# Kernel optimization log

Measured on AMD Instinct MI355X. Metric: run time of the kernel, lower is better.

## Reference

```python
import jax, jax.numpy as jnp
import numpy as np

N = 65536          # flattened input vectors
K = 2048           # num_embeddings (codebook size)
D = 128            # embedding_dim
COMMITMENT_COST = 1.0
DECAY = 0.99
EPS = 1e-05


def setup_inputs() -> dict:
    key = jax.random.key(0)
    k1, k2, k3 = jax.random.split(key, 3)
    inputs = jax.random.normal(k1, (N, D), dtype=jnp.float32)
    embedding = jax.random.normal(k2, (K, D), dtype=jnp.float32) * 0.01
    cluster_size = jnp.zeros((K,), dtype=jnp.float32)
    embed_avg = jax.random.normal(k3, (K, D), dtype=jnp.float32) * 0.01
    return {"inputs": inputs, "embedding": embedding,
            "cluster_size": cluster_size, "embed_avg": embed_avg}


def reference(inputs, embedding, cluster_size, embed_avg):
    input_shape = inputs.shape
    flat = inputs.reshape(-1, D)                                   # [N, D]

    # squared-L2 distances to codebook: [N, K]
    distances = (jnp.sum(flat ** 2, axis=1, keepdims=True)
                 + jnp.sum(embedding ** 2, axis=1)
                 - 2.0 * flat @ embedding.T)
    encoding_indices = jnp.argmin(distances, axis=1)               # [N] int

    quantized = embedding[encoding_indices].reshape(input_shape)   # gather

    # EMA codebook update (training mode). one-hot @ X expressed as segment sums.
    dw = jax.ops.segment_sum(jnp.ones((flat.shape[0],), flat.dtype),
                             encoding_indices, num_segments=K)      # [K]
    new_cluster_size = cluster_size * DECAY + (1.0 - DECAY) * dw
    dw_embed = jax.ops.segment_sum(flat, encoding_indices, num_segments=K)  # [K, D]
    new_embed_avg = embed_avg * DECAY + (1.0 - DECAY) * dw_embed
    n = new_cluster_size.sum()
    smoothed = (new_cluster_size + EPS) / (n + K * EPS) * n
    new_embedding = new_embed_avg / smoothed[:, None]

    # losses (detach == stop_gradient)
    e_latent_loss = jnp.mean((jax.lax.stop_gradient(quantized) - inputs) ** 2)
    q_latent_loss = jnp.mean((quantized - jax.lax.stop_gradient(inputs)) ** 2)
    loss = q_latent_loss + COMMITMENT_COST * e_latent_loss

    # straight-through estimator
    quantized_st = inputs + jax.lax.stop_gradient(quantized - inputs)
    return (quantized_st, loss, encoding_indices,
            new_embedding, new_cluster_size, new_embed_avg)
```

## Files before the change

### kernel.cpp

```cpp
#include <hip/hip_runtime.h>

#define NROWS 65536
#define KCODE 2048
#define DDIM  128

static constexpr float DECAYF = 0.99f;
static constexpr float OMDF   = (float)(1.0 - 0.99);
static constexpr float EPSF   = 1e-5f;
static constexpr float KEPSF  = (float)(2048.0 * 1e-5);
static constexpr float MARGIN = 1e-3f;

typedef __attribute__((ext_vector_type(8))) short bf16x8;
typedef __attribute__((ext_vector_type(4))) float f32x4;

__device__ __forceinline__ unsigned int bf16_rne_bits(float f) {
  unsigned int u = __builtin_bit_cast(unsigned int, f);
  return (u + 0x7fffu + ((u >> 16) & 1u)) >> 16;
}

__global__ __launch_bounds__(256) void k_split(const float* __restrict__ emb,
                                               unsigned short* __restrict__ ehi,
                                               unsigned short* __restrict__ elo) {
  int i = blockIdx.x * 256 + threadIdx.x;
  float f = emb[i];
  unsigned int hr = bf16_rne_bits(f);
  float hif = __builtin_bit_cast(float, hr << 16);
  float lo = f - hif;
  unsigned int lr = bf16_rne_bits(lo);
  ehi[i] = (unsigned short)hr;
  elo[i] = (unsigned short)lr;
}

__global__ __launch_bounds__(256) void k_sumsq_emb(const float* __restrict__ emb,
                                                   float* __restrict__ se) {
#pragma clang fp contract(off)
  int k = blockIdx.x * 256 + threadIdx.x;
  if (k >= KCODE) return;
  const float* row = emb + (size_t)k * DDIM;
  float s = 0.f;
#pragma unroll
  for (int d = 0; d < DDIM; ++d) {
    float q = row[d] * row[d];
    s = s + q;
  }
  se[k] = s;
}

__global__ __launch_bounds__(256, 2) void k_screen(
    const float* __restrict__ x, const unsigned short* __restrict__ ehi,
    const unsigned short* __restrict__ elo, const float* __restrict__ se,
    float* __restrict__ out_idxf, int* __restrict__ idx,
    int* __restrict__ flaglist, int* __restrict__ flagcnt) {
  const int tid = threadIdx.x;
  const int lane = tid & 63;
  const int wid = tid >> 6;
  const int rowbase = (blockIdx.x * 4 + wid) * 32;
  const int l15 = lane & 15, l4 = lane >> 4;

  __shared__ __align__(16) char lds[2][8192];
  char* lbase = &lds[0][0];

  bf16x8 ahi0[4], alo0[4], ahi1[4], alo1[4];
#pragma unroll
  for (int t = 0; t < 2; ++t) {
#pragma unroll
    for (int f = 0; f < 4; ++f) {
      const float4* s4 =
          (const float4*)(x + (size_t)(rowbase + t * 16 + l15) * DDIM + f * 32 + l4 * 8);
      float4 v0 = s4[0], v1 = s4[1];
      float fv[8] = {v0.x, v0.y, v0.z, v0.w, v1.x, v1.y, v1.z, v1.w};
      union { unsigned short u[8]; bf16x8 v; } H, L;
#pragma unroll
      for (int j = 0; j < 8; ++j) {
        unsigned int hr = bf16_rne_bits(fv[j]);
        float hif = __builtin_bit_cast(float, hr << 16);
        unsigned int lr = bf16_rne_bits(fv[j] - hif);
        H.u[j] = (unsigned short)hr;
        L.u[j] = (unsigned short)lr;
      }
      if (t == 0) { ahi0[f] = H.v; alo0[f] = L.v; }
      else        { ahi1[f] = H.v; alo1[f] = L.v; }
    }
  }

  int raddr[2][4];
#pragma unroll
  for (int p = 0; p < 2; ++p)
#pragma unroll
    for (int f = 0; f < 4; ++f)
      raddr[p][f] = p * 4096 + ((l15 * 256 + f * 64 + l4 * 16) ^ ((l15 & 7) << 4));

  const unsigned short* splane = (tid & 128) ? elo : ehi;
  const int po0 = (tid & 127) * 32;
  const char* sp = (const char*)splane + po0;
  const int wplane = (tid >> 7) * 4096;
  const int waddr0 = wplane + (po0 ^ (((po0 >> 8) & 7) << 4));
  const int waddr1 = wplane + ((po0 + 16) ^ ((((po0 + 16) >> 8) & 7) << 4));

  float m1[8], m2[8];
  int k1[8];
#pragma unroll
  for (int s = 0; s < 8; ++s) { m1[s] = INFINITY; m2[s] = INFINITY; k1[s] = 0; }

  {
    int4 v0 = *(const int4*)(sp);
    int4 v1 = *(const int4*)(sp + 16);
    *(int4*)(lbase + waddr0) = v0;
    *(int4*)(lbase + waddr1) = v1;
  }
  __syncthreads();

  int bufoff = 0;
#pragma unroll 2
  for (int g = 0; g < 128; ++g) {
    float sec = se[g * 16 + l15];
    int4 nv0, nv1;
    if (g < 127) {
      nv0 = *(const int4*)(sp + (size_t)(g + 1) * 4096);
      nv1 = *(const int4*)(sp + (size_t)(g + 1) * 4096 + 16);
    }
    f32x4 hh0 = {0.f, 0.f, 0.f, 0.f}, hl0 = {0.f, 0.f, 0.f, 0.f}, lh0 = {0.f, 0.f, 0.f, 0.f};
    f32x4 hh1 = {0.f, 0.f, 0.f, 0.f}, hl1 = {0.f, 0.f, 0.f, 0.f}, lh1 = {0.f, 0.f, 0.f, 0.f};
#pragma unroll
    for (int f = 0; f < 4; ++f) {
      bf16x8 BH = *(const bf16x8*)(lbase + bufoff + raddr[0][f]);
      bf16x8 BL = *(const bf16x8*)(lbase + bufoff + raddr[1][f]);
      hh0 = __builtin_amdgcn_mfma_f32_16x16x32_bf16(ahi0[f], BH, hh0, 0, 0, 0);
      lh0 = __builtin_amdgcn_mfma_f32_16x16x32_bf16(alo0[f], BH, lh0, 0, 0, 0);
      hl0 = __builtin_amdgcn_mfma_f32_16x16x32_bf16(ahi0[f], BL, hl0, 0, 0, 0);
      hh1 = __builtin_amdgcn_mfma_f32_16x16x32_bf16(ahi1[f], BH, hh1, 0, 0, 0);
      lh1 = __builtin_amdgcn_mfma_f32_16x16x32_bf16(alo1[f], BH, lh1, 0, 0, 0);
      hl1 = __builtin_amdgcn_mfma_f32_16x16x32_bf16(ahi1[f], BL, hl1, 0, 0, 0);
    }
    int c_ = g * 16 + l15;
#pragma unroll
    for (int s = 0; s < 4; ++s) {
      float vv = fmaf(-2.f, (hh0[s] + hl0[s]) + lh0[s], sec);
      m2[s] = fminf(m2[s], fmaxf(vv, m1[s]));
      k1[s] = (vv < m1[s]) ? c_ : k1[s];
      m1[s] = fminf(m1[s], vv);
      float vw = fmaf(-2.f, (hh1[s] + hl1[s]) + lh1[s], sec);
      m2[s + 4] = fminf(m2[s + 4], fmaxf(vw, m1[s + 4]));
      k1[s + 4] = (vw < m1[s + 4]) ? c_ : k1[s + 4];
      m1[s + 4] = fminf(m1[s + 4], vw);
    }
    if (g < 127) {
      *(int4*)(lbase + (bufoff ^ 8192) + waddr0) = nv0;
      *(int4*)(lbase + (bufoff ^ 8192) + waddr1) = nv1;
    }
    __syncthreads();
    bufoff ^= 8192;
  }

#pragma unroll
  for (int off = 1; off < 16; off <<= 1) {
#pragma unroll
    for (int s = 0; s < 8; ++s) {
      float om1 = __shfl_xor(m1[s], off);
      float om2 = __shfl_xor(m2[s], off);
      int ok1 = __shfl_xor(k1[s], off);
      m2[s] = fminf(fminf(m2[s], om2), fmaxf(m1[s], om1));
      k1[s] = (om1 < m1[s]) ? ok1 : k1[s];
      m1[s] = fminf(m1[s], om1);
    }
  }
  if (l15 == 0) {
#pragma unroll
    for (int s = 0; s < 8; ++s) {
      int row = rowbase + (s >> 2) * 16 + l4 * 4 + (s & 3);
      idx[row] = k1[s];
      out_idxf[row] = (float)k1[s];
      if (m2[s] - m1[s] <= MARGIN) {
        int p = atomicAdd(flagcnt, 1);
        if (p < NROWS) flaglist[p] = row;
      }
    }
  }
}

__global__ __launch_bounds__(64) void k_exact(
    const float* __restrict__ x, const float* __restrict__ emb,
    const float* __restrict__ se, const int* __restrict__ flaglist,
    const int* __restrict__ flagcnt, int* __restrict__ idx,
    float* __restrict__ out_idxf) {
#pragma clang fp contract(off)
  int cnt = *flagcnt;
  if (cnt > NROWS) cnt = NROWS;
  int lane = threadIdx.x;
  for (int i = blockIdx.x; i < cnt; i += gridDim.x) {
    int row = flaglist[i];
    const float4* xp = (const float4*)(x + (size_t)row * DDIM);
    float4 xr[32];
#pragma unroll
    for (int j = 0; j < 32; ++j) xr[j] = xp[j];
    float sx = 0.f;
#pragma unroll
    for (int j = 0; j < 32; ++j) {
      float q0 = xr[j].x * xr[j].x; sx = sx + q0;
      float q1 = xr[j].y * xr[j].y; sx = sx + q1;
      float q2 = xr[j].z * xr[j].z; sx = sx + q2;
      float q3 = xr[j].w * xr[j].w; sx = sx + q3;
    }
    float bestd = INFINITY;
    int bestk = lane * 32;
    for (int cb = 0; cb < 32; cb += 4) {
      float c4[4] = {0.f, 0.f, 0.f, 0.f};
#pragma unroll
      for (int d4 = 0; d4 < 32; ++d4) {
#pragma unroll
        for (int u = 0; u < 4; ++u) {
          float4 e = ((const float4*)(emb + (size_t)(lane * 32 + cb + u) * DDIM))[d4];
          c4[u] = fmaf(e.x, xr[d4].x, c4[u]);
          c4[u] = fmaf(e.y, xr[d4].y, c4[u]);
          c4[u] = fmaf(e.z, xr[d4].z, c4[u]);
          c4[u] = fmaf(e.w, xr[d4].w, c4[u]);
        }
      }
#pragma unroll
      for (int u = 0; u < 4; ++u) {
        int c = lane * 32 + cb + u;
        float t = sx + se[c];
        float tw = 2.0f * c4[u];
        float d = t - tw;
        if (d < bestd) { bestd = d; bestk = c; }
      }
    }
#pragma unroll
    for (int off = 1; off < 64; off <<= 1) {
      float od = __shfl_xor(bestd, off);
      int ok = __shfl_xor(bestk, off);
      if (od < bestd || (od == bestd && ok < bestk)) { bestd = od; bestk = ok; }
    }
    if (lane == 0) { idx[row] = bestk; out_idxf[row] = (float)bestk; }
  }
}

__global__ __launch_bounds__(256) void k_hist(const int* __restrict__ idx,
                                              int* __restrict__ cnt) {
  int n = blockIdx.x * 256 + threadIdx.x;
  atomicAdd(&cnt[idx[n]], 1);
}

__global__ __launch_bounds__(1024) void k_scan(const int* __restrict__ cnt,
                                               int* __restrict__ off,
                                               int* __restrict__ pos_ctr,
                                               float* __restrict__ dwf) {
  __shared__ int sA[2048], sB[2048];
  int t = threadIdx.x;
  int c0 = cnt[t], c1 = cnt[t + 1024];
  sA[t] = c0; sA[t + 1024] = c1;
  __syncthreads();
  int* src = sA; int* dst = sB;
  for (int o = 1; o < 2048; o <<= 1) {
    int v0 = src[t] + ((t >= o) ? src[t - o] : 0);
    int p1 = t + 1024;
    int v1 = src[p1] + ((p1 >= o) ? src[p1 - o] : 0);
    dst[t] = v0; dst[p1] = v1;
    __syncthreads();
    int* tmp = src; src = dst; dst = tmp;
  }
  int e0 = src[t] - c0;
  int e1 = src[t + 1024] - c1;
  off[t] = e0; off[t + 1024] = e1;
  pos_ctr[t] = e0; pos_ctr[t + 1024] = e1;
  dwf[t] = (float)c0; dwf[t + 1024] = (float)c1;
}

__global__ __launch_bounds__(256) void k_scatter(const int* __restrict__ idx,
                                                 int* __restrict__ pos_ctr,
                                                 int* __restrict__ rowlist) {
  int n = blockIdx.x * 256 + threadIdx.x;
  int k = idx[n];
  int p = atomicAdd(&pos_ctr[k], 1);
  rowlist[p] = n;
}

__global__ __launch_bounds__(128) void k_dwe(const float* __restrict__ x,
                                             const int* __restrict__ rowlist,
                                             const int* __restrict__ cnt,
                                             const int* __restrict__ off,
                                             float* __restrict__ dwe) {
  int k = blockIdx.x, d = threadIdx.x;
  int n = cnt[k], base = off[k];
  float s0 = 0.f, s1 = 0.f, s2 = 0.f, s3 = 0.f;
  int i = 0;
  for (; i + 4 <= n; i += 4) {
    int r0 = rowlist[base + i + 0];
    int r1 = rowlist[base + i + 1];
    int r2 = rowlist[base + i + 2];
    int r3 = rowlist[base + i + 3];
    s0 += x[(size_t)r0 * DDIM + d];
    s1 += x[(size_t)r1 * DDIM + d];
    s2 += x[(size_t)r2 * DDIM + d];
    s3 += x[(size_t)r3 * DDIM + d];
  }
  for (; i < n; ++i) {
    int r = rowlist[base + i];
    s0 += x[(size_t)r * DDIM + d];
  }
  dwe[(size_t)k * DDIM + d] = (s0 + s1) + (s2 + s3);
}

__global__ __launch_bounds__(256) void k_quant2(const float* __restrict__ x,
                                                const float* __restrict__ emb,
                                                const int* __restrict__ idx,
                                                float* __restrict__ out_q,
                                                double* __restrict__ partial_loss) {
#pragma clang fp contract(off)
  int t = blockIdx.x * 256 + threadIdx.x;
  int n = t >> 5, j = t & 31;
  int k = idx[n];
  float4 xv = ((const float4*)(x + (size_t)n * DDIM))[j];
  float4 ev = ((const float4*)(emb + (size_t)k * DDIM))[j];
  float d0 = ev.x - xv.x, d1 = ev.y - xv.y, d2 = ev.z - xv.z, d3 = ev.w - xv.w;
  float4 q;
  q.x = xv.x + d0; q.y = xv.y + d1; q.z = xv.z + d2; q.w = xv.w + d3;
  ((float4*)(out_q + (size_t)n * DDIM))[j] = q;

  float s = d0 * d0 + d1 * d1 + d2 * d2 + d3 * d3;
#pragma unroll
  for (int o = 32; o > 0; o >>= 1) s += __shfl_down(s, o);
  __shared__ float wsum[4];
  if ((threadIdx.x & 63) == 0) wsum[threadIdx.x >> 6] = s;
  __syncthreads();
  if (threadIdx.x == 0)
    partial_loss[blockIdx.x] =
        (double)((wsum[0] + wsum[1]) + (wsum[2] + wsum[3]));
}

__global__ __launch_bounds__(1024) void k_final1(const float* __restrict__ cs,
                                                 const float* __restrict__ dwf,
                                                 float* __restrict__ out_ncs,
                                                 float* __restrict__ smoothed,
                                                 const double* __restrict__ partial_loss,
                                                 float* __restrict__ out_loss) {
#pragma clang fp contract(off)
  __shared__ float red[1024];
  __shared__ double dred[1024];
  int t = threadIdx.x;
  float p0 = cs[t] * DECAYF;
  float p1 = cs[t + 1024] * DECAYF;
  float w0 = OMDF * dwf[t];
  float w1 = OMDF * dwf[t + 1024];
  float ncs0 = p0 + w0;
  float ncs1 = p1 + w1;
  out_ncs[t] = ncs0;
  out_ncs[t + 1024] = ncs1;
  red[t] = ncs0 + ncs1;
  double ds = 0.0;
#pragma unroll
  for (int i = 0; i < 8; ++i) ds += partial_loss[t + i * 1024];
  dred[t] = ds;
  __syncthreads();
  for (int o = 512; o > 0; o >>= 1) {
    if (t < o) { red[t] += red[t + o]; dred[t] += dred[t + o]; }
    __syncthreads();
  }
  float nsum = red[0];
  smoothed[t] = (ncs0 + EPSF) / (nsum + KEPSF) * nsum;
  smoothed[t + 1024] = (ncs1 + EPSF) / (nsum + KEPSF) * nsum;
  if (t == 0) {
    float m = (float)(dred[0] / (double)((size_t)NROWS * DDIM));
    out_loss[0] = m + 1.0f * m;
  }
}

__global__ __launch_bounds__(256) void k_final2(const float* __restrict__ ea,
                                                const float* __restrict__ dwe,
                                                const float* __restrict__ smoothed,
                                                float* __restrict__ out_ne,
                                                float* __restrict__ out_nea) {
#pragma clang fp contract(off)
  int i = blockIdx.x * 256 + threadIdx.x;
  float p = ea[i] * DECAYF;
  float w = OMDF * dwe[i];
  float nea = p + w;
  out_nea[i] = nea;
  out_ne[i] = nea / smoothed[i >> 7];
}

extern "C" void kernel_launch(void* const* d_in, const int* in_sizes, int n_in,
                              void* d_out, int out_size, void* d_ws, size_t ws_size,
                              hipStream_t stream) {
  const float* x   = (const float*)d_in[0];
  const float* emb = (const float*)d_in[1];
  const float* cs  = (const float*)d_in[2];
  const float* ea  = (const float*)d_in[3];

  float* out = (float*)d_out;
  float* out_q    = out;
  float* out_loss = out + 8388608;
  float* out_idx  = out + 8388609;
  float* out_ne   = out + 8454145;
  float* out_ncs  = out + 8716289;
  float* out_nea  = out + 8718337;

  char* ws = (char*)d_ws;
  unsigned short* ehi = (unsigned short*)(ws + 0);
  unsigned short* elo = (unsigned short*)(ws + 524288);
  int*    idx      = (int*)(ws + 1048576);
  int*    flaglist = (int*)(ws + 1310720);
  int*    rowlist  = (int*)(ws + 1572864);
  int*    cnt      = (int*)(ws + 1835008);
  int*    flagcnt  = (int*)(ws + 1843200);
  int*    pos_ctr  = (int*)(ws + 1843264);
  int*    off      = (int*)(ws + 1851456);
  float*  dwf      = (float*)(ws + 1859648);
  float*  se       = (float*)(ws + 1867840);
  float*  smoothed = (float*)(ws + 1876032);
  float*  dwe      = (float*)(ws + 1884224);
  double* partial_loss = (double*)(ws + 2932800);

  hipMemsetAsync(ws + 1835008, 0, 8192 + 64, stream);

  k_split<<<(KCODE * DDIM) / 256, 256, 0, stream>>>(emb, ehi, elo);
  k_sumsq_emb<<<(KCODE + 255) / 256, 256, 0, stream>>>(emb, se);
  k_screen<<<NROWS / 128, 256, 0, stream>>>(x, ehi, elo, se, out_idx, idx, flaglist, flagcnt);
  k_exact<<<2048, 64, 0, stream>>>(x, emb, se, flaglist, flagcnt, idx, out_idx);
  k_hist<<<NROWS / 256, 256, 0, stream>>>(idx, cnt);
  k_scan<<<1, 1024, 0, stream>>>(cnt, off, pos_ctr, dwf);
  k_scatter<<<NROWS / 256, 256, 0, stream>>>(idx, pos_ctr, rowlist);
  k_dwe<<<KCODE, 128, 0, stream>>>(x, rowlist, cnt, off, dwe);
  k_quant2<<<(NROWS * 32) / 256, 256, 0, stream>>>(x, emb, idx, out_q, partial_loss);
  k_final1<<<1, 1024, 0, stream>>>(cs, dwf, out_ncs, smoothed, partial_loss, out_loss);
  k_final2<<<(KCODE * DDIM) / 256, 256, 0, stream>>>(ea, dwe, smoothed, out_ne, out_nea);
}
```

Measured before the change: 408.0 us.

## Tile exact-distance fallback with LDS-staged codebook shared across 16 rows

```diff
diff --git a/kernel.cpp b/kernel.cpp
--- a/kernel.cpp
+++ b/kernel.cpp
@@ -178,7 +178,7 @@
   }
 }
 
-__global__ __launch_bounds__(64) void k_exact(
+__global__ __launch_bounds__(256) void k_exact(
     const float* __restrict__ x, const float* __restrict__ emb,
     const float* __restrict__ se, const int* __restrict__ flaglist,
     const int* __restrict__ flagcnt, int* __restrict__ idx,
@@ -186,52 +186,113 @@
 #pragma clang fp contract(off)
   int cnt = *flagcnt;
   if (cnt > NROWS) cnt = NROWS;
-  int lane = threadIdx.x;
-  for (int i = blockIdx.x; i < cnt; i += gridDim.x) {
-    int row = flaglist[i];
-    const float4* xp = (const float4*)(x + (size_t)row * DDIM);
-    float4 xr[32];
-#pragma unroll
-    for (int j = 0; j < 32; ++j) xr[j] = xp[j];
-    float sx = 0.f;
-#pragma unroll
-    for (int j = 0; j < 32; ++j) {
-      float q0 = xr[j].x * xr[j].x; sx = sx + q0;
-      float q1 = xr[j].y * xr[j].y; sx = sx + q1;
-      float q2 = xr[j].z * xr[j].z; sx = sx + q2;
-      float q3 = xr[j].w * xr[j].w; sx = sx + q3;
-    }
-    float bestd = INFINITY;
-    int bestk = lane * 32;
-    for (int cb = 0; cb < 32; cb += 4) {
-      float c4[4] = {0.f, 0.f, 0.f, 0.f};
+  const int tid = threadIdx.x;
+  const int lane = tid & 63;
+  const int wv = tid >> 6;
+
+  __shared__ __align__(16) float xs[16][128];
+  __shared__ float sxs[16];
+  __shared__ int rids[16];
+  __shared__ __align__(16) float es[64 * 128];
+
+  for (int base = blockIdx.x * 16; base < cnt; base += gridDim.x * 16) {
+    int nrows = cnt - base; if (nrows > 16) nrows = 16;
+    if (tid < 16) rids[tid] = flaglist[base + ((tid < nrows) ? tid : 0)];
+    __syncthreads();
+    {
+      int row = tid >> 4, off = (tid & 15) * 8;
+      const float4* src = (const float4*)(x + (size_t)rids[row] * DDIM + off);
+      float4 a = src[0], b = src[1];
+      *(float4*)&xs[row][off] = a;
+      *(float4*)&xs[row][off + 4] = b;
+    }
+    __syncthreads();
+    if (tid < 16) {
+      float s = 0.f;
+      for (int d = 0; d < DDIM; ++d) { float q = xs[tid][d] * xs[tid][d]; s = s + q; }
+      sxs[tid] = s;
+    }
+    __syncthreads();
+
+    const int row0 = wv * 4;
+    float sxr[4];
+#pragma unroll
+    for (int r = 0; r < 4; ++r) sxr[r] = sxs[row0 + r];
+
+    float bestd[4]; int bestk[4];
+#pragma unroll
+    for (int r = 0; r < 4; ++r) { bestd[r] = INFINITY; bestk[r] = 0; }
+
+    const int ct = tid >> 2;
+    const int d40 = (tid & 3) * 8;
+    for (int tile = 0; tile < 32; ++tile) {
+      float4 ebuf[8];
+      {
+        const float4* esrc =
+            (const float4*)(emb + ((size_t)(tile * 64 + ct)) * DDIM + d40 * 4);
+#pragma unroll
+        for (int j = 0; j < 8; ++j) ebuf[j] = esrc[j];
+      }
+      __syncthreads();
+#pragma unroll
+      for (int j = 0; j < 8; ++j) {
+        int d4 = d40 + j;
+        int slot = d4 ^ (ct & 31);
+        *(float4*)&es[ct * 128 + slot * 4] = ebuf[j];
+      }
+      __syncthreads();
+
+      float a0 = 0.f, a1 = 0.f, a2 = 0.f, a3 = 0.f;
 #pragma unroll
       for (int d4 = 0; d4 < 32; ++d4) {
-#pragma unroll
-        for (int u = 0; u < 4; ++u) {
-          float4 e = ((const float4*)(emb + (size_t)(lane * 32 + cb + u) * DDIM))[d4];
-          c4[u] = fmaf(e.x, xr[d4].x, c4[u]);
-          c4[u] = fmaf(e.y, xr[d4].y, c4[u]);
-          c4[u] = fmaf(e.z, xr[d4].z, c4[u]);
-          c4[u] = fmaf(e.w, xr[d4].w, c4[u]);
+        int slot = d4 ^ (lane & 31);
+        float4 e4 = *(const float4*)&es[lane * 128 + slot * 4];
+        float4 x0 = *(const float4*)&xs[row0 + 0][d4 * 4];
+        float4 x1 = *(const float4*)&xs[row0 + 1][d4 * 4];
+        float4 x2 = *(const float4*)&xs[row0 + 2][d4 * 4];
+        float4 x3 = *(const float4*)&xs[row0 + 3][d4 * 4];
+        a0 = fmaf(e4.x, x0.x, a0); a0 = fmaf(e4.y, x0.y, a0);
+        a0 = fmaf(e4.z, x0.z, a0); a0 = fmaf(e4.w, x0.w, a0);
+        a1 = fmaf(e4.x, x1.x, a1); a1 = fmaf(e4.y, x1.y, a1);
+        a1 = fmaf(e4.z, x1.z, a1); a1 = fmaf(e4.w, x1.w, a1);
+        a2 = fmaf(e4.x, x2.x, a2); a2 = fmaf(e4.y, x2.y, a2);
+        a2 = fmaf(e4.z, x2.z, a2); a2 = fmaf(e4.w, x2.w, a2);
+        a3 = fmaf(e4.x, x3.x, a3); a3 = fmaf(e4.y, x3.y, a3);
+        a3 = fmaf(e4.z, x3.z, a3); a3 = fmaf(e4.w, x3.w, a3);
+      }
+      int code = tile * 64 + lane;
+      float sec = se[code];
+      float acc[4] = {a0, a1, a2, a3};
+#pragma unroll
+      for (int r = 0; r < 4; ++r) {
+        float t_ = sxr[r] + sec;
+        float tw = 2.0f * acc[r];
+        float d_ = t_ - tw;
+        if (d_ < bestd[r]) { bestd[r] = d_; bestk[r] = code; }
+      }
+    }
+
+#pragma unroll
+    for (int off = 1; off < 64; off <<= 1) {
+#pragma unroll
+      for (int r = 0; r < 4; ++r) {
+        float od = __shfl_xor(bestd[r], off);
+        int ok = __shfl_xor(bestk[r], off);
+        if (od < bestd[r] || (od == bestd[r] && ok < bestk[r])) {
+          bestd[r] = od; bestk[r] = ok;
         }
       }
-#pragma unroll
-      for (int u = 0; u < 4; ++u) {
-        int c = lane * 32 + cb + u;
-        float t = sx + se[c];
-        float tw = 2.0f * c4[u];
-        float d = t - tw;
-        if (d < bestd) { bestd = d; bestk = c; }
-      }
-    }
-#pragma unroll
-    for (int off = 1; off < 64; off <<= 1) {
-      float od = __shfl_xor(bestd, off);
-      int ok = __shfl_xor(bestk, off);
-      if (od < bestd || (od == bestd && ok < bestk)) { bestd = od; bestk = ok; }
-    }
-    if (lane == 0) { idx[row] = bestk; out_idxf[row] = (float)bestk; }
+    }
+    if (lane == 0) {
+#pragma unroll
+      for (int r = 0; r < 4; ++r) {
+        if (row0 + r < nrows) {
+          int rid = rids[row0 + r];
+          idx[rid] = bestk[r];
+          out_idxf[rid] = (float)bestk[r];
+        }
+      }
+    }
   }
 }
 
@@ -416,7 +477,7 @@
   k_split<<<(KCODE * DDIM) / 256, 256, 0, stream>>>(emb, ehi, elo);
   k_sumsq_emb<<<(KCODE + 255) / 256, 256, 0, stream>>>(emb, se);
   k_screen<<<NROWS / 128, 256, 0, stream>>>(x, ehi, elo, se, out_idx, idx, flaglist, flagcnt);
-  k_exact<<<2048, 64, 0, stream>>>(x, emb, se, flaglist, flagcnt, idx, out_idx);
+  k_exact<<<128, 256, 0, stream>>>(x, emb, se, flaglist, flagcnt, idx, out_idx);
   k_hist<<<NROWS / 256, 256, 0, stream>>>(idx, cnt);
   k_scan<<<1, 1024, 0, stream>>>(cnt, off, pos_ctr, dwf);
   k_scatter<<<NROWS / 256, 256, 0, stream>>>(idx, pos_ctr, rowlist);
```

After: 402.2 us. About the same (-1.4%).
